# Kernel tuning notes

Measured on AMD Instinct MI355X. Metric: run time of the kernel, lower is better.

Reference implementation:

```python
import jax, jax.numpy as jnp
from jax import lax
import numpy as np

N_FEATURE = 128
EDGE = 12          # int(sqrt(128) + 1)
BATCH = 131072


def maxpool2(x):
    # 2x2 max pool, stride 2, NCHW
    return lax.reduce_window(x, -jnp.inf, lax.max,
                             (1, 1, 2, 2), (1, 1, 2, 2), 'VALID')


def conv3x3(x, w, b):
    # 3x3 conv, padding=1, NCHW / OIHW
    y = lax.conv_general_dilated(x, w, window_strides=(1, 1),
                                 padding=((1, 1), (1, 1)),
                                 dimension_numbers=('NCHW', 'OIHW', 'NCHW'))
    return y + b[None, :, None, None]


def setup_inputs() -> dict:
    key = jax.random.key(0)
    ks = jax.random.split(key, 9)
    x = jax.random.normal(ks[0], (BATCH, N_FEATURE), dtype=jnp.float32)
    conv1_w = jax.random.normal(ks[1], (3, 1, 3, 3), dtype=jnp.float32) * 0.1
    conv1_b = jnp.zeros((3,), dtype=jnp.float32)
    conv2_w = jax.random.normal(ks[2], (6, 3, 3, 3), dtype=jnp.float32) * 0.1
    conv2_b = jnp.zeros((6,), dtype=jnp.float32)
    fc1_w = jax.random.normal(ks[3], (128, 54), dtype=jnp.float32) * 0.1
    fc1_b = jnp.zeros((128,), dtype=jnp.float32)
    out_w = jax.random.normal(ks[4], (N_FEATURE, 128), dtype=jnp.float32) * 0.1
    out_b = jnp.zeros((N_FEATURE,), dtype=jnp.float32)
    return {"x": x, "conv1_w": conv1_w, "conv1_b": conv1_b,
            "conv2_w": conv2_w, "conv2_b": conv2_b,
            "fc1_w": fc1_w, "fc1_b": fc1_b,
            "out_w": out_w, "out_b": out_b}


def reference(x, conv1_w, conv1_b, conv2_w, conv2_b, fc1_w, fc1_b, out_w, out_b):
    num = x.shape[0]
    n = x.shape[1]                       # 128
    pad = EDGE * EDGE - n                # 16 trailing zeros
    # vectorized transto3D: row-major fill of edge x edge grid, zero-padded tail
    g = jnp.pad(x, ((0, 0), (0, pad))).reshape(num, 1, EDGE, EDGE)
    h = jax.nn.relu(maxpool2(conv3x3(g, conv1_w, conv1_b)))      # [num,3,6,6]
    h = jax.nn.relu(maxpool2(conv3x3(h, conv2_w, conv2_b)))      # [num,6,3,3]
    h = h.reshape(num, 54)
    h = jax.nn.relu(h @ fc1_w.T + fc1_b)                         # [num,128]
    return h @ out_w.T + out_b                                   # [num,128]
```

## Files before the change

kernel.cpp:

```cpp
#include <hip/hip_runtime.h>

typedef unsigned int uint;
typedef unsigned short ushort;

using bf16x8 = __attribute__((ext_vector_type(8))) short;
using f32x4  = __attribute__((ext_vector_type(4))) float;

__device__ __forceinline__ float b2f(ushort u) {
  union { uint i; float f; } v; v.i = ((uint)u) << 16; return v.f;
}
__device__ __forceinline__ ushort f2b(float f) {
  union { float f; uint i; } v; v.f = f;
  uint r = (v.i + 0x7fffu + ((v.i >> 16) & 1u)) >> 16;
  return (ushort)r;
}
__device__ __forceinline__ bf16x8 ldfrag(const ushort* p) {
  union { uint4 u; bf16x8 v; } x; x.u = *(const uint4*)p; return x.v;
}

__global__ __launch_bounds__(256, 1) void conv_kernel(
    const float* __restrict__ x,
    const float* __restrict__ w1g, const float* __restrict__ b1g,
    const float* __restrict__ w2g, const float* __restrict__ b2g,
    ushort* __restrict__ h2ws) {
  const int s = blockIdx.x * 256 + threadIdx.x;
  const float* xs = x + (size_t)s * 128;

  float xv[128];
#pragma unroll
  for (int i = 0; i < 32; ++i) {
    const float4 v = ((const float4*)xs)[i];
    xv[4 * i + 0] = v.x; xv[4 * i + 1] = v.y;
    xv[4 * i + 2] = v.z; xv[4 * i + 3] = v.w;
  }
#pragma unroll
  for (int i = 0; i < 128; ++i) asm("" : "+v"(xv[i]));

  float w1[3][9], b1[3];
#pragma unroll
  for (int c = 0; c < 3; ++c) {
    b1[c] = b1g[c];
#pragma unroll
    for (int q = 0; q < 9; ++q) w1[c][q] = w1g[c * 9 + q];
  }

  float h1[3][6][6];
#pragma unroll
  for (int pr = 0; pr < 6; ++pr)
#pragma unroll
    for (int pc = 0; pc < 6; ++pc)
#pragma unroll
      for (int ch = 0; ch < 3; ++ch) {
        float m = -3.0e38f;
#pragma unroll
        for (int dr = 0; dr < 2; ++dr)
#pragma unroll
          for (int dc = 0; dc < 2; ++dc) {
            float a = 0.f;
#pragma unroll
            for (int ky = 0; ky < 3; ++ky)
#pragma unroll
              for (int kx = 0; kx < 3; ++kx) {
                const int r = 2 * pr + dr + ky - 1;
                const int c = 2 * pc + dc + kx - 1;
                if (r >= 0 && r < 12 && c >= 0 && c < 12 && (12 * r + c) < 128)
                  a = fmaf(w1[ch][ky * 3 + kx], xv[12 * r + c], a);
              }
            m = fmaxf(m, a);
          }
        h1[ch][pr][pc] = fmaxf(m + b1[ch], 0.f);
      }

  float h2[54];
#pragma unroll
  for (int o = 0; o < 6; ++o) {
    float w2[27];
#pragma unroll
    for (int q = 0; q < 27; ++q) w2[q] = w2g[o * 27 + q];
    const float bo = b2g[o];
#pragma unroll
    for (int qr = 0; qr < 3; ++qr)
#pragma unroll
      for (int qc = 0; qc < 3; ++qc) {
        float m = -3.0e38f;
#pragma unroll
        for (int dr = 0; dr < 2; ++dr)
#pragma unroll
          for (int dc = 0; dc < 2; ++dc) {
            float a = 0.f;
#pragma unroll
            for (int i = 0; i < 3; ++i)
#pragma unroll
              for (int ky = 0; ky < 3; ++ky)
#pragma unroll
                for (int kx = 0; kx < 3; ++kx) {
                  const int yy = 2 * qr + dr + ky - 1;
                  const int xx = 2 * qc + dc + kx - 1;
                  if (yy >= 0 && yy < 6 && xx >= 0 && xx < 6)
                    a = fmaf(w2[i * 9 + ky * 3 + kx], h1[i][yy][xx], a);
                }
            m = fmaxf(m, a);
          }
        h2[o * 9 + qr * 3 + qc] = fmaxf(m + bo, 0.f);
      }
  }

  uint pk[32];
#pragma unroll
  for (int q = 0; q < 27; ++q)
    pk[q] = (uint)f2b(h2[2 * q]) | ((uint)f2b(h2[2 * q + 1]) << 16);
#pragma unroll
  for (int q = 27; q < 32; ++q) pk[q] = 0u;
  uint4* dst = (uint4*)(h2ws + (size_t)s * 64);
#pragma unroll
  for (int i = 0; i < 8; ++i) {
    uint4 v; v.x = pk[4 * i]; v.y = pk[4 * i + 1];
    v.z = pk[4 * i + 2]; v.w = pk[4 * i + 3];
    dst[i] = v;
  }
}

__global__ __launch_bounds__(256, 2) void fc_kernel(
    const ushort* __restrict__ h2ws,
    const float* __restrict__ fc1w, const float* __restrict__ fc1b,
    const float* __restrict__ outw, const float* __restrict__ outb,
    float* __restrict__ out) {
  __shared__ __align__(16) union {
    struct { ushort h2s[128][72]; ushort w1s[128][72]; } p1;
    struct { ushort tA[128][132]; ushort owB[128][132]; } p2;
  } U;
  __shared__ __align__(16) float fb1[128];
  __shared__ __align__(16) float ob[128];

  const int t = threadIdx.x;
  const int s0 = blockIdx.x * 128;
  const int lane = t & 63, wv = t >> 6;
  const int quad = lane >> 4, lm = lane & 15;

  if (t < 128) { fb1[t] = fc1b[t]; ob[t] = outb[t]; }

#pragma unroll
  for (int i = 0; i < 4; ++i) {
    const int f = t + 256 * i;
    const int si = f >> 3, kb = f & 7;
    *(uint4*)&U.p1.h2s[si][kb * 8] =
        *(const uint4*)(h2ws + (size_t)(s0 + si) * 64 + kb * 8);
  }
#pragma unroll
  for (int i = 0; i < 27; ++i) {
    const int f = t + 256 * i;
    const int n = f / 54, k = f - 54 * n;
    U.p1.w1s[n][k] = f2b(fc1w[f]);
  }
  if (t < 128) {
    uint* p = (uint*)&U.p1.w1s[t][54];
#pragma unroll
    for (int q = 0; q < 5; ++q) p[q] = 0u;
  }
  __syncthreads();

  f32x4 acc[2][8];
#pragma unroll
  for (int mt = 0; mt < 2; ++mt)
#pragma unroll
    for (int st = 0; st < 8; ++st) acc[mt][st] = (f32x4){0.f, 0.f, 0.f, 0.f};

#pragma unroll
  for (int kk = 0; kk < 2; ++kk) {
    const int ko = kk * 32 + quad * 8;
    bf16x8 aw[2], bh[8];
#pragma unroll
    for (int mt = 0; mt < 2; ++mt)
      aw[mt] = ldfrag(&U.p1.w1s[32 * wv + 16 * mt + lm][ko]);
#pragma unroll
    for (int st = 0; st < 8; ++st)
      bh[st] = ldfrag(&U.p1.h2s[16 * st + lm][ko]);
#pragma unroll
    for (int mt = 0; mt < 2; ++mt)
#pragma unroll
      for (int st = 0; st < 8; ++st)
        acc[mt][st] = __builtin_amdgcn_mfma_f32_16x16x32_bf16(
            aw[mt], bh[st], acc[mt][st], 0, 0, 0);
  }
  __syncthreads();

#pragma unroll
  for (int mt = 0; mt < 2; ++mt) {
    const int jb = 32 * wv + 16 * mt + quad * 4;
    const float4 bj = *(const float4*)&fb1[jb];
#pragma unroll
    for (int st = 0; st < 8; ++st) {
      const int sR = 16 * st + lm;
      const float v0 = fmaxf(acc[mt][st][0] + bj.x, 0.f);
      const float v1 = fmaxf(acc[mt][st][1] + bj.y, 0.f);
      const float v2 = fmaxf(acc[mt][st][2] + bj.z, 0.f);
      const float v3 = fmaxf(acc[mt][st][3] + bj.w, 0.f);
      uint2 pv;
      pv.x = (uint)f2b(v0) | ((uint)f2b(v1) << 16);
      pv.y = (uint)f2b(v2) | ((uint)f2b(v3) << 16);
      *(uint2*)&U.p2.tA[sR][jb] = pv;
    }
  }
#pragma unroll
  for (int i = 0; i < 16; ++i) {
    const int f = t + 256 * i;
    const int o = f >> 5, j4 = (f & 31) * 4;
    const float4 v = *(const float4*)(outw + o * 128 + j4);
    uint2 pv;
    pv.x = (uint)f2b(v.x) | ((uint)f2b(v.y) << 16);
    pv.y = (uint)f2b(v.z) | ((uint)f2b(v.w) << 16);
    *(uint2*)&U.p2.owB[o][j4] = pv;
  }
  __syncthreads();

  f32x4 acc2[2][8];
#pragma unroll
  for (int mt = 0; mt < 2; ++mt)
#pragma unroll
    for (int st = 0; st < 8; ++st) acc2[mt][st] = (f32x4){0.f, 0.f, 0.f, 0.f};

#pragma unroll
  for (int kk = 0; kk < 4; ++kk) {
    const int ko = kk * 32 + quad * 8;
    bf16x8 ao[2], bt[8];
#pragma unroll
    for (int mt = 0; mt < 2; ++mt)
      ao[mt] = ldfrag(&U.p2.owB[32 * wv + 16 * mt + lm][ko]);
#pragma unroll
    for (int st = 0; st < 8; ++st)
      bt[st] = ldfrag(&U.p2.tA[16 * st + lm][ko]);
#pragma unroll
    for (int mt = 0; mt < 2; ++mt)
#pragma unroll
      for (int st = 0; st < 8; ++st)
        acc2[mt][st] = __builtin_amdgcn_mfma_f32_16x16x32_bf16(
            ao[mt], bt[st], acc2[mt][st], 0, 0, 0);
  }

#pragma unroll
  for (int mt = 0; mt < 2; ++mt) {
    const int obase = 32 * wv + 16 * mt + quad * 4;
    const float4 b4 = *(const float4*)&ob[obase];
#pragma unroll
    for (int st = 0; st < 8; ++st) {
      const int srow = s0 + 16 * st + lm;
      float4 o4;
      o4.x = acc2[mt][st][0] + b4.x;
      o4.y = acc2[mt][st][1] + b4.y;
      o4.z = acc2[mt][st][2] + b4.z;
      o4.w = acc2[mt][st][3] + b4.w;
      *(float4*)&out[(size_t)srow * 128 + obase] = o4;
    }
  }
}

extern "C" void kernel_launch(void* const* d_in, const int* in_sizes, int n_in,
                              void* d_out, int out_size, void* d_ws, size_t ws_size,
                              hipStream_t stream) {
  const float* x    = (const float*)d_in[0];
  const float* w1   = (const float*)d_in[1];
  const float* b1   = (const float*)d_in[2];
  const float* w2   = (const float*)d_in[3];
  const float* b2   = (const float*)d_in[4];
  const float* fc1w = (const float*)d_in[5];
  const float* fc1b = (const float*)d_in[6];
  const float* outw = (const float*)d_in[7];
  const float* outb = (const float*)d_in[8];
  float* outp = (float*)d_out;
  ushort* ws  = (ushort*)d_ws;

  const int N = in_sizes[0] / 128;

  conv_kernel<<<N / 256, 256, 0, stream>>>(x, w1, b1, w2, b2, ws);
  fc_kernel<<<N / 128, 256, 0, stream>>>(ws, fc1w, fc1b, outw, outb, outp);
}
```

Measured before the change: 185.2 us.

## Load FC operands directly into registers, shrink LDS, raise fc occupancy

The fc kernel now loads h2 activation fragments straight from global memory into MFMA B-registers, and loads out_w fragments from global and converts them to bf16 in registers, instead of staging both through LDS. This removes the h2s and owB shared buffers and one barrier, cutting LDS use so launch bounds can ask for 3 blocks per CU. The trade-off is more register pressure and uncoalesced, repeated global reads of out_w per wave, with its float-to-bf16 conversion now done redundantly by every block.

```diff
diff --git a/kernel.cpp b/kernel.cpp
--- a/kernel.cpp
+++ b/kernel.cpp
@@ -16,6 +16,14 @@
 }
 __device__ __forceinline__ bf16x8 ldfrag(const ushort* p) {
   union { uint4 u; bf16x8 v; } x; x.u = *(const uint4*)p; return x.v;
+}
+__device__ __forceinline__ bf16x8 pack8(const float4 a, const float4 b) {
+  union { uint4 u; bf16x8 v; } x;
+  x.u.x = (uint)f2b(a.x) | ((uint)f2b(a.y) << 16);
+  x.u.y = (uint)f2b(a.z) | ((uint)f2b(a.w) << 16);
+  x.u.z = (uint)f2b(b.x) | ((uint)f2b(b.y) << 16);
+  x.u.w = (uint)f2b(b.z) | ((uint)f2b(b.w) << 16);
+  return x.v;
 }
 
 __global__ __launch_bounds__(256, 1) void conv_kernel(
@@ -120,15 +128,13 @@
   }
 }
 
-__global__ __launch_bounds__(256, 2) void fc_kernel(
+__global__ __launch_bounds__(256, 3) void fc_kernel(
     const ushort* __restrict__ h2ws,
     const float* __restrict__ fc1w, const float* __restrict__ fc1b,
     const float* __restrict__ outw, const float* __restrict__ outb,
     float* __restrict__ out) {
-  __shared__ __align__(16) union {
-    struct { ushort h2s[128][72]; ushort w1s[128][72]; } p1;
-    struct { ushort tA[128][132]; ushort owB[128][132]; } p2;
-  } U;
+  __shared__ __align__(16) ushort w1s[128][72];
+  __shared__ __align__(16) ushort tA[128][132];
   __shared__ __align__(16) float fb1[128];
   __shared__ __align__(16) float ob[128];
 
@@ -137,23 +143,24 @@
   const int lane = t & 63, wv = t >> 6;
   const int quad = lane >> 4, lm = lane & 15;
 
+  bf16x8 bh[2][8];
+#pragma unroll
+  for (int st = 0; st < 8; ++st) {
+    const ushort* rp = h2ws + (size_t)(s0 + 16 * st + lm) * 64 + quad * 8;
+    bh[0][st] = ldfrag(rp);
+    bh[1][st] = ldfrag(rp + 32);
+  }
+
   if (t < 128) { fb1[t] = fc1b[t]; ob[t] = outb[t]; }
 
-#pragma unroll
-  for (int i = 0; i < 4; ++i) {
-    const int f = t + 256 * i;
-    const int si = f >> 3, kb = f & 7;
-    *(uint4*)&U.p1.h2s[si][kb * 8] =
-        *(const uint4*)(h2ws + (size_t)(s0 + si) * 64 + kb * 8);
-  }
 #pragma unroll
   for (int i = 0; i < 27; ++i) {
     const int f = t + 256 * i;
     const int n = f / 54, k = f - 54 * n;
-    U.p1.w1s[n][k] = f2b(fc1w[f]);
+    w1s[n][k] = f2b(fc1w[f]);
   }
   if (t < 128) {
-    uint* p = (uint*)&U.p1.w1s[t][54];
+    uint* p = (uint*)&w1s[t][54];
 #pragma unroll
     for (int q = 0; q < 5; ++q) p[q] = 0u;
   }
@@ -168,21 +175,17 @@
 #pragma unroll
   for (int kk = 0; kk < 2; ++kk) {
     const int ko = kk * 32 + quad * 8;
-    bf16x8 aw[2], bh[8];
+    bf16x8 aw[2];
 #pragma unroll
     for (int mt = 0; mt < 2; ++mt)
-      aw[mt] = ldfrag(&U.p1.w1s[32 * wv + 16 * mt + lm][ko]);
-#pragma unroll
-    for (int st = 0; st < 8; ++st)
-      bh[st] = ldfrag(&U.p1.h2s[16 * st + lm][ko]);
+      aw[mt] = ldfrag(&w1s[32 * wv + 16 * mt + lm][ko]);
 #pragma unroll
     for (int mt = 0; mt < 2; ++mt)
 #pragma unroll
       for (int st = 0; st < 8; ++st)
         acc[mt][st] = __builtin_amdgcn_mfma_f32_16x16x32_bf16(
-            aw[mt], bh[st], acc[mt][st], 0, 0, 0);
-  }
-  __syncthreads();
+            aw[mt], bh[kk][st], acc[mt][st], 0, 0, 0);
+  }
 
 #pragma unroll
   for (int mt = 0; mt < 2; ++mt) {
@@ -198,18 +201,8 @@
       uint2 pv;
       pv.x = (uint)f2b(v0) | ((uint)f2b(v1) << 16);
       pv.y = (uint)f2b(v2) | ((uint)f2b(v3) << 16);
-      *(uint2*)&U.p2.tA[sR][jb] = pv;
+      *(uint2*)&tA[sR][jb] = pv;
     }
-  }
-#pragma unroll
-  for (int i = 0; i < 16; ++i) {
-    const int f = t + 256 * i;
-    const int o = f >> 5, j4 = (f & 31) * 4;
-    const float4 v = *(const float4*)(outw + o * 128 + j4);
-    uint2 pv;
-    pv.x = (uint)f2b(v.x) | ((uint)f2b(v.y) << 16);
-    pv.y = (uint)f2b(v.z) | ((uint)f2b(v.w) << 16);
-    *(uint2*)&U.p2.owB[o][j4] = pv;
   }
   __syncthreads();
 
@@ -224,11 +217,15 @@
     const int ko = kk * 32 + quad * 8;
     bf16x8 ao[2], bt[8];
 #pragma unroll
-    for (int mt = 0; mt < 2; ++mt)
-      ao[mt] = ldfrag(&U.p2.owB[32 * wv + 16 * mt + lm][ko]);
+    for (int mt = 0; mt < 2; ++mt) {
+      const float* rp = outw + (size_t)(32 * wv + 16 * mt + lm) * 128 + ko;
+      const float4 v0 = *(const float4*)rp;
+      const float4 v1 = *(const float4*)(rp + 4);
+      ao[mt] = pack8(v0, v1);
+    }
 #pragma unroll
     for (int st = 0; st < 8; ++st)
-      bt[st] = ldfrag(&U.p2.tA[16 * st + lm][ko]);
+      bt[st] = ldfrag(&tA[16 * st + lm][ko]);
 #pragma unroll
     for (int mt = 0; mt < 2; ++mt)
 #pragma unroll
```

Result: faster. 178.7 us (-3.5%).
